# Optimization experiments

Measured on AMD Instinct MI355X. Metric: run time of the kernel, lower is better.

Reference implementation:

```python
import jax, jax.numpy as jnp
import numpy as np

STOP_IX, CONTINUE_IX = 0, 1


def setup_inputs() -> dict:
    key = jax.random.key(0)
    B, T, b, A = 64, 512, 64, 18
    ks = jax.random.split(key, 5)
    # normalized log-probabilities, as produced by the abstract policy net
    stop_logps = jax.nn.log_softmax(jax.random.normal(ks[0], (B, T + 1, b, 2)), axis=-1)
    start_logps = jax.nn.log_softmax(jax.random.normal(ks[1], (B, T + 1, b)), axis=-1)
    action_logps = jax.nn.log_softmax(jax.random.normal(ks[2], (B, T + 1, b, A)), axis=-1)
    actions = jax.random.randint(ks[3], (B, T), 0, A)
    lengths = jax.random.randint(ks[4], (B,), 1, T + 1)  # traj length in [1, T]
    return dict(stop_logps=stop_logps, start_logps=start_logps,
                action_logps=action_logps, actions=actions, lengths=lengths)


def reference(stop_logps, start_logps, action_logps, actions, lengths):
    B, Tp1, b, _ = stop_logps.shape
    T = Tp1 - 1
    # chosen action logps per (batch, step, option): (B, T, b)
    chosen = jnp.take_along_axis(action_logps[:, :T], actions[:, :, None, None], axis=3)[..., 0]
    beta = stop_logps[..., STOP_IX]        # (B, T+1, b) log p(stop)
    ombeta = stop_logps[..., CONTINUE_IX]  # (B, T+1, b) log p(continue)
    eye = jnp.eye(b, dtype=bool)

    # f_0: all mass on option 0 (log prob 0)
    f0 = jnp.full((B, b), -jnp.inf, dtype=stop_logps.dtype).at[:, 0].set(0.0)

    def step(f_prev, xs):
        beta_i, ombeta_i, start_i, chosen_i = xs  # each (B, b)
        # trans[k,i,j] = logaddexp(beta_i + start_j, [i==j] * one_minus_beta_i)
        bs = beta_i[:, :, None] + start_i[:, None, :]  # (B, b, b)
        trans = jnp.where(eye[None], jnp.logaddexp(bs, ombeta_i[:, :, None]), bs)
        f_new = jax.nn.logsumexp(f_prev[:, :, None] + trans + chosen_i[:, None, :], axis=1)
        return f_new, f_new

    # per-step inputs for i = 1 .. T-1, time-major: (T-1, B, b)
    xs = (jnp.moveaxis(beta[:, 1:T], 0, 1),
          jnp.moveaxis(ombeta[:, 1:T], 0, 1),
          jnp.moveaxis(start_logps[:, 1:T], 0, 1),
          jnp.moveaxis(chosen[:, 1:T], 0, 1))
    _, fs = jax.lax.scan(step, f0, xs)
    f_all = jnp.concatenate([f0[None], fs], axis=0)  # (T, B, b)

    batch_ix = jnp.arange(B)
    x0 = f_all[lengths - 1, batch_ix]                 # (B, b)
    x1 = stop_logps[batch_ix, lengths, :, STOP_IX]    # (B, b)
    total_logps = jax.nn.logsumexp(x0 + x1, axis=1)   # (B,)
    return -jnp.sum(total_logps)
```

## Files before the change

### kernel.cpp

```cpp
#include <hip/hip_runtime.h>


#define CH   8
#define WARM 16
#define CLEN 64
#define SLOT 16

template <int CTRL, int RMASK>
__device__ __forceinline__ float dpp_add(float x) {
    int yi = __builtin_amdgcn_update_dpp(
        0, __builtin_bit_cast(int, x), CTRL, RMASK, 0xf, true);
    return x + __builtin_bit_cast(float, yi);
}

__device__ __forceinline__ float wave_sum64(float x) {
    x = dpp_add<0x111, 0xf>(x);
    x = dpp_add<0x112, 0xf>(x);
    x = dpp_add<0x114, 0xf>(x);
    x = dpp_add<0x118, 0xf>(x);
    x = dpp_add<0x142, 0xa>(x);
    x = dpp_add<0x143, 0xc>(x);
    return __builtin_bit_cast(float,
        __builtin_amdgcn_readlane(__builtin_bit_cast(int, x), 63));
}

__global__ __launch_bounds__(256)
void hmm_gather(const float* __restrict__ act,
                const int*   __restrict__ actions,
                const int*   __restrict__ lengths,
                float* __restrict__ chosen,
                int T, int A)
{
    const int b = blockIdx.y;
    const int L = lengths[b];
    const int i = blockIdx.x * 256 + threadIdx.x;
    const int t = i >> 6;
    if (t >= T || t >= L) return;
    const int k = i & 63;
    const int a = actions[(size_t)b * T + t];
    chosen[((size_t)b * T + t) * 64 + k] =
        act[(((size_t)b * (T + 1) + t) * 64 + k) * A + a];
}

template <bool PG>
__global__ __launch_bounds__(64)
void hmm_fwd(const float* __restrict__ stop,
             const float* __restrict__ start,
             const float* __restrict__ act,
             const int*   __restrict__ actions,
             const int*   __restrict__ lengths,
             const float* __restrict__ chosen,
             float* __restrict__ ws,
             int T, int A, int NC)
{
    const int bi   = blockIdx.x;
    const int c    = blockIdx.y;
    const int lane = threadIdx.x;
    const int Tp1  = T + 1;
    const int NB   = 64;
    const int rowA = NB * A;

    const int L = lengths[bi];
    const int a = 1 + c * CLEN;
    const int cstar = (L >= 2) ? ((L - 2) / CLEN) : 0;
    if (c > cstar) return;

    const int t_end = min(L, a + CLEN);
    const int t0    = (c == 0) ? 1 : (a - WARM);
    const int n     = t_end - t0;
    const int nwarm = a - t0;

    const float* stopB  = stop  + (size_t)bi * Tp1 * NB * 2;
    const float* startB = start + (size_t)bi * Tp1 * NB;
    const float* actB   = act   + (size_t)bi * Tp1 * NB * A;
    const int*   actsB  = actions + (size_t)bi * T;

    __shared__ int offL[CLEN + WARM + CH];
    if constexpr (!PG) {
        for (int i = lane; i < n + CH; i += 64) {
            const int tt = min(t0 + i, t_end - 1);
            offL[i] = tt * rowA + actsB[tt];
        }
    }

    float p = (c == 0) ? ((lane == 0) ? 1.0f : 0.0f) : 1.0f;
    float slast   = 1.0f;
    float warmcap = 0.0f;
    float Eshift  = 0.0f;

    const float* spL = stopB  + (size_t)t0 * (NB * 2) + lane * 2;
    const float* stL = startB + (size_t)t0 * NB + lane;
    const float* chL = PG ? (chosen + ((size_t)bi * T + t0) * NB + lane)
                          : (const float*)nullptr;
    const int laneA = lane * A;

    float bB[2][CH], bO[2][CH], bS[2][CH], bC[2][CH];

#define LOADF(SL, j) do {                                                    \
    const float* sp  = spL + (size_t)(j) * (CH * NB * 2);                    \
    const float* st2 = stL + (size_t)(j) * (CH * NB);                        \
    _Pragma("unroll")                                                        \
    for (int i = 0; i < CH; ++i) {                                           \
        if constexpr (PG)                                                    \
            bC[SL][i] = chL[((size_t)((j) * CH + i)) * NB];                  \
        else                                                                 \
            bC[SL][i] = actB[offL[(j) * CH + i] + laneA];                    \
        const float2 so = *(const float2*)(sp + i * (NB * 2));               \
        bB[SL][i] = so.x;                                                    \
        bO[SL][i] = so.y;                                                    \
        bS[SL][i] = st2[i * NB];                                             \
    } } while (0)

#define LOADC(SL, j) do {                                                    \
    _Pragma("unroll")                                                        \
    for (int i = 0; i < CH; ++i) {                                           \
        const int tt = min(t0 + (j) * CH + i, t_end - 1);                    \
        if constexpr (PG)                                                    \
            bC[SL][i] = chosen[((size_t)bi * T + tt) * NB + lane];           \
        else                                                                 \
            bC[SL][i] = actB[offL[(j) * CH + i] + laneA];                    \
        const float2 so = *(const float2*)(stopB + (size_t)tt * (NB * 2)     \
                                           + lane * 2);                      \
        bB[SL][i] = so.x;                                                    \
        bO[SL][i] = so.y;                                                    \
        bS[SL][i] = startB[(size_t)tt * NB + lane];                          \
    } } while (0)

#define LOAD(SL, j) do {                                                     \
    if (((j) + 1) * CH <= n) LOADF(SL, j); else LOADC(SL, j); } while (0)

#define COMPUTE(SL, j) do {                                                  \
    _Pragma("unroll")                                                        \
    for (int i = 0; i < CH; ++i) {                                           \
        if ((j) * CH + i < n) {                                              \
            const float e1 = __expf(bC[SL][i] + bS[SL][i]);                  \
            const float e2 = __expf(bC[SL][i] + bO[SL][i]);                  \
            const float eb = __expf(bB[SL][i]);                              \
            const float q  = e2 * p;                 \
            const float s  = wave_sum64(p * eb);                             \
            slast = s;                                                       \
            if ((j) * CH + i == nwarm - 1)                                   \
                warmcap = __log2f(s) + Eshift;                               \
            p = fmaf(e1, s, q);                                              \
        }                                                                    \
    }                                                                        \
                                  \
    {                                                                        \
        const unsigned sb = __builtin_bit_cast(unsigned, slast);             \
        const int ef = (int)(sb >> 23);                 \
        const float sc = __builtin_bit_cast(float,                           \
                             (unsigned)(254 - ef) << 23);   \
        p *= sc;                                                             \
        slast *= sc;                                                         \
        Eshift += (float)(ef - 127);                                         \
    } } while (0)

    const int nch = (n + CH - 1) / CH;
    if (n > 0) {
        int j = 0;
        LOAD(0, 0);
        while (true) {
            if (j + 1 < nch) LOAD(1, j + 1);
            COMPUTE(0, j);
            ++j; if (j >= nch) break;
            if (j + 1 < nch) LOAD(0, j + 1);
            COMPUTE(1, j);
            ++j; if (j >= nch) break;
        }
    }

    float C2;
    if (c == cstar) {
        const float bl = stopB[(size_t)L * (NB * 2) + lane * 2];
        const float s  = wave_sum64(p * __expf(bl));
        C2 = __log2f(s) + Eshift - warmcap;
    } else {
        C2 = __log2f(slast) + Eshift - warmcap;
    }

    if (lane == 0)
        ws[(size_t)bi * NC + c] = C2;

#undef LOADF
#undef LOADC
#undef LOAD
#undef COMPUTE
}

__global__ __launch_bounds__(64)
void hmm_reduce(const float* __restrict__ ws,
                const int*   __restrict__ lengths,
                float* __restrict__ out, int B, int NC)
{
    const int lane = threadIdx.x;
    float acc = 0.0f;
    for (int b = lane; b < B; b += 64) {
        const int L = lengths[b];
        const int cstar = (L >= 2) ? ((L - 2) / CLEN) : 0;
        float s = 0.0f;
        for (int c = 0; c <= cstar; ++c)
            s += ws[(size_t)b * NC + c];
        acc += s;
    }
    const float tot = wave_sum64(acc);
    if (lane == 0)
        out[0] = -0.69314718055994531f * tot;
}

extern "C" void kernel_launch(void* const* d_in, const int* in_sizes, int n_in,
                              void* d_out, int out_size, void* d_ws, size_t ws_size,
                              hipStream_t stream)
{
    const float* stop    = (const float*)d_in[0];
    const float* start   = (const float*)d_in[1];
    const float* act     = (const float*)d_in[2];
    const int*   actions = (const int*)d_in[3];
    const int*   lengths = (const int*)d_in[4];
    float* out = (float*)d_out;
    float* ws  = (float*)d_ws;

    const int B   = in_sizes[4];
    const int T   = in_sizes[3] / B;
    const int Tp1 = T + 1;
    const int A   = in_sizes[2] / (B * Tp1 * 64);

    int NC = (T - 1 + CLEN - 1) / CLEN;
    if (NC < 1) NC = 1;

    const size_t partial_floats = (((size_t)B * NC) + 63) & ~(size_t)63;
    const size_t chosen_bytes   = (size_t)B * T * 64 * sizeof(float);
    const bool   pg = (ws_size >= partial_floats * sizeof(float) + chosen_bytes);
    float* chosen = ws + partial_floats;

    if (pg) {
        hmm_gather<<<dim3((T * 64 + 255) / 256, B), dim3(256), 0, stream>>>(
            act, actions, lengths, chosen, T, A);
        hmm_fwd<true><<<dim3(B, NC), dim3(64), 0, stream>>>(
            stop, start, act, actions, lengths, chosen, ws, T, A, NC);
    } else {
        hmm_fwd<false><<<dim3(B, NC), dim3(64), 0, stream>>>(
            stop, start, act, actions, lengths, nullptr, ws, T, A, NC);
    }
    hmm_reduce<<<dim3(1), dim3(64), 0, stream>>>(ws, lengths, out, B, NC);
}
```

Before: 227.3 us.

## Fuse gather, forward chunks and reduction into one cooperative kernel

Replaces the three separate launches (gather, chunked forward, reduce) with a single cooperative kernel that uses grid-wide syncs between phases. The gather phase is redistributed across all waves, with 4-row unrolled non-temporal loads. The chunk length is halved, doubling the number of parallel chunks per batch row at the cost of more warm-up overhead per chunk. The three-kernel path remains as a fallback if the cooperative launch fails. The aim is to remove launch gaps and tail effects, but grid syncs add their own cost and the one-wave blocks may limit gather throughput.

```diff
diff --git a/kernel.cpp b/kernel.cpp
--- a/kernel.cpp
+++ b/kernel.cpp
@@ -1,10 +1,13 @@
 #include <hip/hip_runtime.h>
+#include <hip/hip_cooperative_groups.h>
+
+namespace cg = cooperative_groups;
 
 
 #define CH   8
 #define WARM 16
-#define CLEN 64
-#define SLOT 16
+#define CLEN 32
+#define NB   64
 
 template <int CTRL, int RMASK>
 __device__ __forceinline__ float dpp_add(float x) {
@@ -24,40 +27,45 @@
         __builtin_amdgcn_readlane(__builtin_bit_cast(int, x), 63));
 }
 
-__global__ __launch_bounds__(256)
-void hmm_gather(const float* __restrict__ act,
-                const int*   __restrict__ actions,
-                const int*   __restrict__ lengths,
-                float* __restrict__ chosen,
-                int T, int A)
-{
-    const int b = blockIdx.y;
-    const int L = lengths[b];
-    const int i = blockIdx.x * 256 + threadIdx.x;
-    const int t = i >> 6;
-    if (t >= T || t >= L) return;
-    const int k = i & 63;
-    const int a = actions[(size_t)b * T + t];
-    chosen[((size_t)b * T + t) * 64 + k] =
-        act[(((size_t)b * (T + 1) + t) * 64 + k) * A + a];
+
+__device__ __forceinline__ void gather_phase(
+    const float* __restrict__ act, const int* __restrict__ actions,
+    const int* __restrict__ lengths, float* __restrict__ chosen,
+    int B, int T, int A, int waveId, int nWaves, int lane)
+{
+    const int nrows = B * T;
+    for (int r0 = waveId * 4; r0 < nrows; r0 += nWaves * 4) {
+        float  v[4]; size_t dst[4]; bool ok[4];
+#pragma unroll
+        for (int u = 0; u < 4; ++u) {
+            const int r = r0 + u;
+            ok[u] = false;
+            if (r < nrows) {
+                const int b = r / T;
+                const int t = r - b * T;
+                if (t < lengths[b]) {
+                    const int a = actions[r];
+                    v[u] = __builtin_nontemporal_load(
+                        act + (((size_t)b * (T + 1) + t) * NB + lane) * A + a);
+                    dst[u] = (size_t)r * NB + lane;
+                    ok[u] = true;
+                }
+            }
+        }
+#pragma unroll
+        for (int u = 0; u < 4; ++u)
+            if (ok[u]) chosen[dst[u]] = v[u];
+    }
 }
 
 template <bool PG>
-__global__ __launch_bounds__(64)
-void hmm_fwd(const float* __restrict__ stop,
-             const float* __restrict__ start,
-             const float* __restrict__ act,
-             const int*   __restrict__ actions,
-             const int*   __restrict__ lengths,
-             const float* __restrict__ chosen,
-             float* __restrict__ ws,
-             int T, int A, int NC)
-{
-    const int bi   = blockIdx.x;
-    const int c    = blockIdx.y;
-    const int lane = threadIdx.x;
+__device__ __forceinline__ void fwd_chunk(
+    const float* __restrict__ stop, const float* __restrict__ start,
+    const float* __restrict__ act, const int* __restrict__ actions,
+    const int* __restrict__ lengths, const float* __restrict__ chosen,
+    float* __restrict__ ws, int T, int A, int NC, int bi, int c, int lane)
+{
     const int Tp1  = T + 1;
-    const int NB   = 64;
     const int rowA = NB * A;
 
     const int L = lengths[bi];
@@ -187,18 +195,16 @@
 #undef COMPUTE
 }
 
-__global__ __launch_bounds__(64)
-void hmm_reduce(const float* __restrict__ ws,
-                const int*   __restrict__ lengths,
-                float* __restrict__ out, int B, int NC)
-{
-    const int lane = threadIdx.x;
+__device__ __forceinline__ void reduce_phase(
+    const float* __restrict__ ws, const int* __restrict__ lengths,
+    float* __restrict__ out, int B, int NC, int lane)
+{
     float acc = 0.0f;
     for (int b = lane; b < B; b += 64) {
         const int L = lengths[b];
-        const int cstar = (L >= 2) ? ((L - 2) / CLEN) : 0;
+        const int cs = (L >= 2) ? ((L - 2) / CLEN) : 0;
         float s = 0.0f;
-        for (int c = 0; c <= cstar; ++c)
+        for (int c = 0; c <= cs; ++c)
             s += ws[(size_t)b * NC + c];
         acc += s;
     }
@@ -206,6 +212,67 @@
     if (lane == 0)
         out[0] = -0.69314718055994531f * tot;
 }
+
+
+__global__ __launch_bounds__(64)
+void hmm_fused(const float* __restrict__ stop, const float* __restrict__ start,
+               const float* __restrict__ act, const int* __restrict__ actions,
+               const int* __restrict__ lengths, float* __restrict__ chosen,
+               float* __restrict__ ws, float* __restrict__ out,
+               int T, int A, int NC, int B)
+{
+    const int lane   = threadIdx.x;
+    const int waveId = blockIdx.x * gridDim.y + blockIdx.y;
+    const int nWaves = gridDim.x * gridDim.y;
+
+    gather_phase(act, actions, lengths, chosen, B, T, A, waveId, nWaves, lane);
+    __threadfence();
+    cg::this_grid().sync();
+
+    fwd_chunk<true>(stop, start, act, actions, lengths, chosen, ws,
+                    T, A, NC, blockIdx.x, blockIdx.y, lane);
+    __threadfence();
+    cg::this_grid().sync();
+
+    if (blockIdx.x == 0 && blockIdx.y == 0)
+        reduce_phase(ws, lengths, out, B, NC, lane);
+}
+
+
+__global__ __launch_bounds__(256)
+void hmm_gather(const float* __restrict__ act, const int* __restrict__ actions,
+                const int* __restrict__ lengths, float* __restrict__ chosen,
+                int T, int A)
+{
+    const int b = blockIdx.y;
+    const int L = lengths[b];
+    const int i = blockIdx.x * 256 + threadIdx.x;
+    const int t = i >> 6;
+    if (t >= T || t >= L) return;
+    const int k = i & 63;
+    const int a = actions[(size_t)b * T + t];
+    chosen[((size_t)b * T + t) * 64 + k] =
+        act[(((size_t)b * (T + 1) + t) * 64 + k) * A + a];
+}
+
+template <bool PG>
+__global__ __launch_bounds__(64)
+void hmm_fwd(const float* __restrict__ stop, const float* __restrict__ start,
+             const float* __restrict__ act, const int* __restrict__ actions,
+             const int* __restrict__ lengths, const float* __restrict__ chosen,
+             float* __restrict__ ws, int T, int A, int NC)
+{
+    fwd_chunk<PG>(stop, start, act, actions, lengths, chosen, ws,
+                  T, A, NC, blockIdx.x, blockIdx.y, threadIdx.x);
+}
+
+__global__ __launch_bounds__(64)
+void hmm_reduce(const float* __restrict__ ws, const int* __restrict__ lengths,
+                float* __restrict__ out, int B, int NC)
+{
+    reduce_phase(ws, lengths, out, B, NC, threadIdx.x);
+}
+
 
 extern "C" void kernel_launch(void* const* d_in, const int* in_sizes, int n_in,
                               void* d_out, int out_size, void* d_ws, size_t ws_size,
@@ -232,14 +299,28 @@
     const bool   pg = (ws_size >= partial_floats * sizeof(float) + chosen_bytes);
     float* chosen = ws + partial_floats;
 
+    bool done = false;
     if (pg) {
-        hmm_gather<<<dim3((T * 64 + 255) / 256, B), dim3(256), 0, stream>>>(
-            act, actions, lengths, chosen, T, A);
-        hmm_fwd<true><<<dim3(B, NC), dim3(64), 0, stream>>>(
-            stop, start, act, actions, lengths, chosen, ws, T, A, NC);
-    } else {
-        hmm_fwd<false><<<dim3(B, NC), dim3(64), 0, stream>>>(
-            stop, start, act, actions, lengths, nullptr, ws, T, A, NC);
-    }
-    hmm_reduce<<<dim3(1), dim3(64), 0, stream>>>(ws, lengths, out, B, NC);
-}
+        void* args[] = {
+            (void*)&stop, (void*)&start, (void*)&act, (void*)&actions,
+            (void*)&lengths, (void*)&chosen, (void*)&ws, (void*)&out,
+            (void*)&T, (void*)&A, (void*)&NC, (void*)&B };
+        const hipError_t e = hipLaunchCooperativeKernel(
+            reinterpret_cast<const void*>(hmm_fused),
+            dim3(B, NC), dim3(64), args, 0, stream);
+        done = (e == hipSuccess);
+    }
+
+    if (!done) {
+        if (pg) {
+            hmm_gather<<<dim3((T * 64 + 255) / 256, B), dim3(256), 0, stream>>>(
+                act, actions, lengths, chosen, T, A);
+            hmm_fwd<true><<<dim3(B, NC), dim3(64), 0, stream>>>(
+                stop, start, act, actions, lengths, chosen, ws, T, A, NC);
+        } else {
+            hmm_fwd<false><<<dim3(B, NC), dim3(64), 0, stream>>>(
+                stop, start, act, actions, lengths, nullptr, ws, T, A, NC);
+        }
+        hmm_reduce<<<dim3(1), dim3(64), 0, stream>>>(ws, lengths, out, B, NC);
+    }
+}
```

New measurement: 546.9 us. +140.6%, slower.

## Drop gather pre-pass, halve chunk length, triple-buffer per-step loads

Applied to the files above, without the earlier changes.

Removes the separate gather kernel that materialized chosen action log-probs, so the forward kernel always reads the action values directly through shared-memory offsets. Chunk length drops from 64 to 32, doubling the number of independent time chunks per sequence for more parallelism at the cost of more warm-up overhead per chunk. The load pipeline moves from double to triple buffering to hide more global-load latency, using more registers in exchange.

```diff
diff --git a/kernel.cpp b/kernel.cpp
--- a/kernel.cpp
+++ b/kernel.cpp
@@ -3,8 +3,8 @@
 
 #define CH   8
 #define WARM 16
-#define CLEN 64
-#define SLOT 16
+#define CLEN 32
+#define NB   64
 
 template <int CTRL, int RMASK>
 __device__ __forceinline__ float dpp_add(float x) {
@@ -24,32 +24,12 @@
         __builtin_amdgcn_readlane(__builtin_bit_cast(int, x), 63));
 }
 
-__global__ __launch_bounds__(256)
-void hmm_gather(const float* __restrict__ act,
-                const int*   __restrict__ actions,
-                const int*   __restrict__ lengths,
-                float* __restrict__ chosen,
-                int T, int A)
-{
-    const int b = blockIdx.y;
-    const int L = lengths[b];
-    const int i = blockIdx.x * 256 + threadIdx.x;
-    const int t = i >> 6;
-    if (t >= T || t >= L) return;
-    const int k = i & 63;
-    const int a = actions[(size_t)b * T + t];
-    chosen[((size_t)b * T + t) * 64 + k] =
-        act[(((size_t)b * (T + 1) + t) * 64 + k) * A + a];
-}
-
-template <bool PG>
 __global__ __launch_bounds__(64)
 void hmm_fwd(const float* __restrict__ stop,
              const float* __restrict__ start,
              const float* __restrict__ act,
              const int*   __restrict__ actions,
              const int*   __restrict__ lengths,
-             const float* __restrict__ chosen,
              float* __restrict__ ws,
              int T, int A, int NC)
 {
@@ -57,7 +37,6 @@
     const int c    = blockIdx.y;
     const int lane = threadIdx.x;
     const int Tp1  = T + 1;
-    const int NB   = 64;
     const int rowA = NB * A;
 
     const int L = lengths[bi];
@@ -76,11 +55,9 @@
     const int*   actsB  = actions + (size_t)bi * T;
 
     __shared__ int offL[CLEN + WARM + CH];
-    if constexpr (!PG) {
-        for (int i = lane; i < n + CH; i += 64) {
-            const int tt = min(t0 + i, t_end - 1);
-            offL[i] = tt * rowA + actsB[tt];
-        }
+    for (int i = lane; i < n + CH; i += 64) {
+        const int tt = min(t0 + i, t_end - 1);
+        offL[i] = tt * rowA + actsB[tt];
     }
 
     float p = (c == 0) ? ((lane == 0) ? 1.0f : 0.0f) : 1.0f;
@@ -90,21 +67,16 @@
 
     const float* spL = stopB  + (size_t)t0 * (NB * 2) + lane * 2;
     const float* stL = startB + (size_t)t0 * NB + lane;
-    const float* chL = PG ? (chosen + ((size_t)bi * T + t0) * NB + lane)
-                          : (const float*)nullptr;
     const int laneA = lane * A;
 
-    float bB[2][CH], bO[2][CH], bS[2][CH], bC[2][CH];
+    float bB[3][CH], bO[3][CH], bS[3][CH], bC[3][CH];
 
 #define LOADF(SL, j) do {                                                    \
     const float* sp  = spL + (size_t)(j) * (CH * NB * 2);                    \
     const float* st2 = stL + (size_t)(j) * (CH * NB);                        \
     _Pragma("unroll")                                                        \
     for (int i = 0; i < CH; ++i) {                                           \
-        if constexpr (PG)                                                    \
-            bC[SL][i] = chL[((size_t)((j) * CH + i)) * NB];                  \
-        else                                                                 \
-            bC[SL][i] = actB[offL[(j) * CH + i] + laneA];                    \
+        bC[SL][i] = actB[offL[(j) * CH + i] + laneA];                        \
         const float2 so = *(const float2*)(sp + i * (NB * 2));               \
         bB[SL][i] = so.x;                                                    \
         bO[SL][i] = so.y;                                                    \
@@ -114,11 +86,8 @@
 #define LOADC(SL, j) do {                                                    \
     _Pragma("unroll")                                                        \
     for (int i = 0; i < CH; ++i) {                                           \
+        bC[SL][i] = actB[offL[(j) * CH + i] + laneA];                        \
         const int tt = min(t0 + (j) * CH + i, t_end - 1);                    \
-        if constexpr (PG)                                                    \
-            bC[SL][i] = chosen[((size_t)bi * T + tt) * NB + lane];           \
-        else                                                                 \
-            bC[SL][i] = actB[offL[(j) * CH + i] + laneA];                    \
         const float2 so = *(const float2*)(stopB + (size_t)tt * (NB * 2)     \
                                            + lane * 2);                      \
         bB[SL][i] = so.x;                                                    \
@@ -157,14 +126,18 @@
 
     const int nch = (n + CH - 1) / CH;
     if (n > 0) {
+        LOAD(0, 0);
+        if (nch > 1) LOAD(1, 1);
         int j = 0;
-        LOAD(0, 0);
         while (true) {
-            if (j + 1 < nch) LOAD(1, j + 1);
+            if (j + 2 < nch) LOAD(2, j + 2);
             COMPUTE(0, j);
             ++j; if (j >= nch) break;
-            if (j + 1 < nch) LOAD(0, j + 1);
+            if (j + 2 < nch) LOAD(0, j + 2);
             COMPUTE(1, j);
+            ++j; if (j >= nch) break;
+            if (j + 2 < nch) LOAD(1, j + 2);
+            COMPUTE(2, j);
             ++j; if (j >= nch) break;
         }
     }
@@ -196,9 +169,9 @@
     float acc = 0.0f;
     for (int b = lane; b < B; b += 64) {
         const int L = lengths[b];
-        const int cstar = (L >= 2) ? ((L - 2) / CLEN) : 0;
+        const int cs = (L >= 2) ? ((L - 2) / CLEN) : 0;
         float s = 0.0f;
-        for (int c = 0; c <= cstar; ++c)
+        for (int c = 0; c <= cs; ++c)
             s += ws[(size_t)b * NC + c];
         acc += s;
     }
@@ -227,19 +200,7 @@
     int NC = (T - 1 + CLEN - 1) / CLEN;
     if (NC < 1) NC = 1;
 
-    const size_t partial_floats = (((size_t)B * NC) + 63) & ~(size_t)63;
-    const size_t chosen_bytes   = (size_t)B * T * 64 * sizeof(float);
-    const bool   pg = (ws_size >= partial_floats * sizeof(float) + chosen_bytes);
-    float* chosen = ws + partial_floats;
-
-    if (pg) {
-        hmm_gather<<<dim3((T * 64 + 255) / 256, B), dim3(256), 0, stream>>>(
-            act, actions, lengths, chosen, T, A);
-        hmm_fwd<true><<<dim3(B, NC), dim3(64), 0, stream>>>(
-            stop, start, act, actions, lengths, chosen, ws, T, A, NC);
-    } else {
-        hmm_fwd<false><<<dim3(B, NC), dim3(64), 0, stream>>>(
-            stop, start, act, actions, lengths, nullptr, ws, T, A, NC);
-    }
+    hmm_fwd<<<dim3(B, NC), dim3(64), 0, stream>>>(
+        stop, start, act, actions, lengths, ws, T, A, NC);
     hmm_reduce<<<dim3(1), dim3(64), 0, stream>>>(ws, lengths, out, B, NC);
 }
```

New measurement: 221.3 us. -2.6%, faster.
